# Kernel tuning notes

Hardware: AMD Instinct MI355X
Metric: run time of the kernel (lower is better)

The kernel has to match this reference:

```python
import jax, jax.numpy as jnp
import numpy as np

N = 1_000_000
C = 64
H = Wd = 2048
EPS = 1e-5


def _build_neighbors(seed=0):
    """Active-site neighbor map for a 3x3 submanifold conv on an HxW grid.
    Returns int32 [N, 9]; entry = index of active neighbor site, or -1."""
    rng = np.random.default_rng(seed)
    flat = rng.permutation(H * Wd)[:N]            # unique active coords
    grid = np.full(H * Wd, -1, np.int64)
    grid[flat] = np.arange(N)
    ys, xs = flat // Wd, flat % Wd
    cols = []
    for dy in (-1, 0, 1):
        for dx in (-1, 0, 1):
            ny, nx = ys + dy, xs + dx
            valid = (ny >= 0) & (ny < H) & (nx >= 0) & (nx < Wd)
            nf = np.where(valid, np.clip(ny, 0, H - 1) * Wd + np.clip(nx, 0, Wd - 1), 0)
            nb = np.where(valid, grid[nf], -1)    # -1 also if neighbor inactive
            cols.append(nb)
    return np.stack(cols, axis=1).astype(np.int32)


def setup_inputs() -> dict:
    key = jax.random.key(0)
    k1, k2, k3 = jax.random.split(key, 3)
    scale = 1.0 / np.sqrt(9 * C)
    return {
        "features": jax.random.normal(k1, (N, C), jnp.float32),
        "neighbor": jnp.asarray(_build_neighbors()),
        "W1": jax.random.normal(k2, (9, C, C), jnp.float32) * scale,
        "gamma1": jnp.ones((C,), jnp.float32),
        "beta1": jnp.zeros((C,), jnp.float32),
        "W2": jax.random.normal(k3, (9, C, C), jnp.float32) * scale,
        "gamma2": jnp.ones((C,), jnp.float32),
        "beta2": jnp.zeros((C,), jnp.float32),
    }


def _subm_conv(f, W, neighbor):
    # gather -> per-tap GEMM -> accumulate (submanifold: outputs only at active sites)
    out = jnp.zeros_like(f)
    for k in range(9):
        idx = neighbor[:, k]
        mask = (idx >= 0)
        g = jnp.where(mask[:, None], f[jnp.maximum(idx, 0)], 0.0)  # [N, C]
        out = out + g @ W[k]
    return out


def _bn(f, gamma, beta):
    # BatchNorm1d over the active-site axis (training-mode batch statistics)
    m = f.mean(axis=0)
    v = f.var(axis=0)
    return (f - m) * jax.lax.rsqrt(v + EPS) * gamma + beta


def reference(features, neighbor, W1, gamma1, beta1, W2, gamma2, beta2):
    out = _subm_conv(features, W1, neighbor)
    out = jax.nn.relu(_bn(out, gamma1, beta1))
    out = _subm_conv(out, W2, neighbor)
    out = _bn(out, gamma2, beta2) + features
    return jax.nn.relu(out)
```

## Files before the change

kernel.cpp:

```cpp
#include <hip/hip_runtime.h>

#define NSITES 1000000
#define CCH 64
#define EPS_BN 1e-5f

typedef __bf16 bf16x8 __attribute__((ext_vector_type(8)));
typedef float f32x4 __attribute__((ext_vector_type(4)));
typedef unsigned short ushort_t;

__device__ __forceinline__ unsigned short f2bf(float x) {
    __bf16 h = (__bf16)x;
    return __builtin_bit_cast(unsigned short, h);
}
__device__ __forceinline__ float bf2f(unsigned short u) {
    return (float)__builtin_bit_cast(__bf16, u);
}

__global__ void cast_kernel(const float* __restrict__ f, ushort_t* __restrict__ o, int total16) {
    int stride = gridDim.x * blockDim.x;
    for (int i = blockIdx.x * blockDim.x + threadIdx.x; i < total16; i += stride) {
        const float4* fp = (const float4*)(f + (size_t)i * 16);
        float4 v0 = fp[0];
        float4 v1 = fp[1];
        float4 v2 = fp[2];
        float4 v3 = fp[3];
        uint4 pa, pb;
        ushort_t* up = (ushort_t*)&pa;
        up[0] = f2bf(v0.x); up[1] = f2bf(v0.y); up[2] = f2bf(v0.z); up[3] = f2bf(v0.w);
        up[4] = f2bf(v1.x); up[5] = f2bf(v1.y); up[6] = f2bf(v1.z); up[7] = f2bf(v1.w);
        ushort_t* uq = (ushort_t*)&pb;
        uq[0] = f2bf(v2.x); uq[1] = f2bf(v2.y); uq[2] = f2bf(v2.z); uq[3] = f2bf(v2.w);
        uq[4] = f2bf(v3.x); uq[5] = f2bf(v3.y); uq[6] = f2bf(v3.z); uq[7] = f2bf(v3.w);
        uint4* op = (uint4*)(o + (size_t)i * 16);
        op[0] = pa;
        op[1] = pb;
    }
}

__global__ void swizzle_kernel(const float* __restrict__ W1, const float* __restrict__ W2,
                               ushort_t* __restrict__ W1s, ushort_t* __restrict__ W2s) {
    int t = blockIdx.x * blockDim.x + threadIdx.x;
    const float* Wg = W1;
    ushort_t* dst = W1s;
    int u = t;
    if (t >= 36864) { Wg = W2; dst = W2s; u = t - 36864; }
    int j = u & 7;
    int lane = (u >> 3) & 63;
    int nt = (u >> 9) & 3;
    int kk = (u >> 11) & 1;
    int tap = u >> 12;
    int k = 32 * kk + 8 * (lane >> 4) + j;
    int n = 16 * nt + (lane & 15);
    dst[u] = f2bf(Wg[tap * 4096 + k * 64 + n]);
}

__device__ __forceinline__ void gatherA(const ushort_t* __restrict__ fin,
                                        const int (&idxr)[2][9], int t, int quad,
                                        uint4 (&dst)[2][2]) {
#pragma unroll
    for (int mt = 0; mt < 2; ++mt) {
        int id = idxr[mt][t];
        int r = (id < 0) ? NSITES : id;
        const uint4* p = (const uint4*)(fin + ((size_t)r << 6) + (quad << 3));
        dst[mt][0] = p[0];
        dst[mt][1] = p[4];
    }
}

__device__ __forceinline__ void loadB(const ushort_t* __restrict__ Wsw, int t, int kk, int lane,
                                      bf16x8 (&B)[4]) {
#pragma unroll
    for (int nt = 0; nt < 4; ++nt)
        B[nt] = *(const bf16x8*)(Wsw + (size_t)(((t * 2 + kk) * 4 + nt) * 64 + lane) * 8);
}

template <bool OUT_BF16>
__global__ __launch_bounds__(256) void conv_kernel(
    const ushort_t* __restrict__ fin,
    const int* __restrict__ nbr,
    const ushort_t* __restrict__ Wsw,
    ushort_t* __restrict__ out_bf, float* __restrict__ out_f,
    float* __restrict__ s_sum, float* __restrict__ s_sq) {

    __shared__ float bs_sum[64];
    __shared__ float bs_sq[64];

    const int tid  = threadIdx.x;
    const int wv   = tid >> 6;
    const int lane = tid & 63;
    const int quad = lane >> 4;
    const int l15  = lane & 15;
    const int sbase = blockIdx.x * 128 + wv * 32;

    if (tid < 64) { bs_sum[tid] = 0.f; bs_sq[tid] = 0.f; }
    __syncthreads();

    int idxr[2][9];
#pragma unroll
    for (int mt = 0; mt < 2; ++mt) {
        int s = sbase + mt * 16 + l15;
        int sc = (s < NSITES) ? s : 0;
        bool sv = (s < NSITES);
#pragma unroll
        for (int t = 0; t < 9; ++t) {
            int id = nbr[(size_t)sc * 9 + t];
            idxr[mt][t] = sv ? id : -1;
        }
    }

    f32x4 acc[2][4];
#pragma unroll
    for (int mt = 0; mt < 2; ++mt)
#pragma unroll
        for (int nt = 0; nt < 4; ++nt) acc[mt][nt] = (f32x4){0.f, 0.f, 0.f, 0.f};

    uint4 abuf[3][2][2];
    gatherA(fin, idxr, 0, quad, abuf[0]);
    gatherA(fin, idxr, 1, quad, abuf[1]);

    bf16x8 B0[4];
    loadB(Wsw, 0, 0, lane, B0);

#pragma unroll
    for (int t = 0; t < 9; ++t) {
        bf16x8 B1[4];
        loadB(Wsw, t, 1, lane, B1);

        if (t < 7) gatherA(fin, idxr, t + 2, quad, abuf[(t + 2) % 3]);

        bf16x8 B0n[4];
        if (t < 8) loadB(Wsw, t + 1, 0, lane, B0n);

        __builtin_amdgcn_s_setprio(1);
#pragma unroll
        for (int mt = 0; mt < 2; ++mt) {
            bf16x8 a0 = __builtin_bit_cast(bf16x8, abuf[t % 3][mt][0]);
#pragma unroll
            for (int nt = 0; nt < 4; ++nt)
                acc[mt][nt] = __builtin_amdgcn_mfma_f32_16x16x32_bf16(a0, B0[nt], acc[mt][nt], 0, 0, 0);
        }
#pragma unroll
        for (int mt = 0; mt < 2; ++mt) {
            bf16x8 a1 = __builtin_bit_cast(bf16x8, abuf[t % 3][mt][1]);
#pragma unroll
            for (int nt = 0; nt < 4; ++nt)
                acc[mt][nt] = __builtin_amdgcn_mfma_f32_16x16x32_bf16(a1, B1[nt], acc[mt][nt], 0, 0, 0);
        }
        __builtin_amdgcn_s_setprio(0);

        if (t < 8) {
#pragma unroll
            for (int nt = 0; nt < 4; ++nt) B0[nt] = B0n[nt];
        }
    }

    float ss[4] = {0.f, 0.f, 0.f, 0.f};
    float sq[4] = {0.f, 0.f, 0.f, 0.f};
#pragma unroll
    for (int mt = 0; mt < 2; ++mt)
#pragma unroll
        for (int nt = 0; nt < 4; ++nt)
#pragma unroll
            for (int r = 0; r < 4; ++r) {
                float v = acc[mt][nt][r];
                ss[nt] += v;
                sq[nt] += v * v;
            }
#pragma unroll
    for (int nt = 0; nt < 4; ++nt) {
        ss[nt] += __shfl_xor(ss[nt], 16);
        ss[nt] += __shfl_xor(ss[nt], 32);
        sq[nt] += __shfl_xor(sq[nt], 16);
        sq[nt] += __shfl_xor(sq[nt], 32);
    }
    if (lane < 16) {
#pragma unroll
        for (int nt = 0; nt < 4; ++nt) {
            atomicAdd(&bs_sum[nt * 16 + l15], ss[nt]);
            atomicAdd(&bs_sq[nt * 16 + l15], sq[nt]);
        }
    }

    if constexpr (OUT_BF16) {
        __shared__ ushort_t tr[4 * 32 * 72];
        ushort_t* w_tr = tr + wv * 32 * 72;
#pragma unroll
        for (int mt = 0; mt < 2; ++mt)
#pragma unroll
            for (int nt = 0; nt < 4; ++nt)
#pragma unroll
                for (int r = 0; r < 4; ++r)
                    w_tr[(mt * 16 + 4 * quad + r) * 72 + nt * 16 + l15] = f2bf(acc[mt][nt][r]);
        int site_s = lane >> 1;
        int half = lane & 1;
        int gs = sbase + site_s;
        if (gs < NSITES) {
#pragma unroll
            for (int c = 0; c < 4; ++c) {
                uint4 d = *(const uint4*)(w_tr + site_s * 72 + half * 32 + c * 8);
                *(uint4*)(out_bf + (size_t)gs * 64 + half * 32 + c * 8) = d;
            }
        }
    } else {
#pragma unroll
        for (int mt = 0; mt < 2; ++mt)
#pragma unroll
            for (int nt = 0; nt < 4; ++nt)
#pragma unroll
                for (int r = 0; r < 4; ++r) {
                    int site = sbase + mt * 16 + 4 * quad + r;
                    if (site < NSITES)
                        out_f[(size_t)site * 64 + nt * 16 + l15] = acc[mt][nt][r];
                }
    }

    __syncthreads();
    if (tid < 64) {
        atomicAdd(&s_sum[tid], bs_sum[tid]);
        atomicAdd(&s_sq[tid], bs_sq[tid]);
    }
}

__global__ void finalize_kernel(const float* __restrict__ sum, const float* __restrict__ sq,
                                const float* __restrict__ gamma, const float* __restrict__ beta,
                                float* __restrict__ a, float* __restrict__ b) {
    int c = threadIdx.x;
    const float invn = 1.0f / (float)NSITES;
    float m = sum[c] * invn;
    float v = sq[c] * invn - m * m;
    float s = gamma[c] * rsqrtf(v + EPS_BN);
    a[c] = s;
    b[c] = beta[c] - m * s;
}

__global__ void act_kernel(ushort_t* __restrict__ h, const float* __restrict__ a,
                           const float* __restrict__ b, int total16) {
    int stride = gridDim.x * blockDim.x;
    for (int i = blockIdx.x * blockDim.x + threadIdx.x; i < total16; i += stride) {
        int c16 = (i & 3) * 16;
        uint4* hp = (uint4*)(h + (size_t)i * 16);
        uint4 v0 = hp[0];
        uint4 v1 = hp[1];
        float av[16], bv[16];
#pragma unroll
        for (int q = 0; q < 4; ++q) {
            *(float4*)&av[q * 4] = *(const float4*)(a + c16 + q * 4);
            *(float4*)&bv[q * 4] = *(const float4*)(b + c16 + q * 4);
        }
        ushort_t* up = (ushort_t*)&v0;
#pragma unroll
        for (int j = 0; j < 8; ++j) {
            float x = bf2f(up[j]);
            up[j] = f2bf(fmaxf(av[j] * x + bv[j], 0.f));
        }
        ushort_t* uq = (ushort_t*)&v1;
#pragma unroll
        for (int j = 0; j < 8; ++j) {
            float x = bf2f(uq[j]);
            uq[j] = f2bf(fmaxf(av[8 + j] * x + bv[8 + j], 0.f));
        }
        hp[0] = v0;
        hp[1] = v1;
    }
}

__global__ void residual_kernel(float* __restrict__ out, const float* __restrict__ feat,
                                const float* __restrict__ a2, const float* __restrict__ b2,
                                int total8) {
    int stride = gridDim.x * blockDim.x;
    for (int i = blockIdx.x * blockDim.x + threadIdx.x; i < total8; i += stride) {
        float4* op = (float4*)(out + (size_t)i * 8);
        const float4* fp = (const float4*)(feat + (size_t)i * 8);
        float4 h0 = op[0];
        float4 h1v = op[1];
        float4 f0 = fp[0];
        float4 f1 = fp[1];
        int c8 = (i & 7) * 8;
        float4 av0 = *(const float4*)(a2 + c8);
        float4 av1 = *(const float4*)(a2 + c8 + 4);
        float4 bv0 = *(const float4*)(b2 + c8);
        float4 bv1 = *(const float4*)(b2 + c8 + 4);
        float4 r0, r1;
        r0.x = fmaxf(av0.x * h0.x + bv0.x + f0.x, 0.f);
        r0.y = fmaxf(av0.y * h0.y + bv0.y + f0.y, 0.f);
        r0.z = fmaxf(av0.z * h0.z + bv0.z + f0.z, 0.f);
        r0.w = fmaxf(av0.w * h0.w + bv0.w + f0.w, 0.f);
        r1.x = fmaxf(av1.x * h1v.x + bv1.x + f1.x, 0.f);
        r1.y = fmaxf(av1.y * h1v.y + bv1.y + f1.y, 0.f);
        r1.z = fmaxf(av1.z * h1v.z + bv1.z + f1.z, 0.f);
        r1.w = fmaxf(av1.w * h1v.w + bv1.w + f1.w, 0.f);
        op[0] = r0;
        op[1] = r1;
    }
}

extern "C" void kernel_launch(void* const* d_in, const int* in_sizes, int n_in,
                              void* d_out, int out_size, void* d_ws, size_t ws_size,
                              hipStream_t stream) {
    const float* features = (const float*)d_in[0];
    const int* nbr        = (const int*)d_in[1];
    const float* W1       = (const float*)d_in[2];
    const float* gamma1   = (const float*)d_in[3];
    const float* beta1    = (const float*)d_in[4];
    const float* W2       = (const float*)d_in[5];
    const float* gamma2   = (const float*)d_in[6];
    const float* beta2    = (const float*)d_in[7];

    char* ws = (char*)d_ws;
    const size_t NB = (size_t)NSITES * CCH * sizeof(unsigned short);

    ushort_t* fbf = (ushort_t*)d_out;
    ushort_t* h1  = (ushort_t*)ws;
    size_t off = NB + 512;
    ushort_t* W1s = (ushort_t*)(ws + off);
    ushort_t* W2s = (ushort_t*)(ws + off + 147456);
    float* stats  = (float*)(ws + off + 294912);
    float* ab     = (float*)(ws + off + 294912 + 1024);

    hipMemsetAsync(stats, 0, 256 * sizeof(float), stream);
    hipMemsetAsync(fbf + (size_t)NSITES * 64, 0, 128, stream);
    hipMemsetAsync(h1 + (size_t)NSITES * 64, 0, 128, stream);

    cast_kernel<<<8192, 256, 0, stream>>>(features, fbf, NSITES * CCH / 16);
    swizzle_kernel<<<288, 256, 0, stream>>>(W1, W2, W1s, W2s);

    const int nblk = (NSITES + 127) / 128;
    conv_kernel<true><<<nblk, 256, 0, stream>>>(
        fbf, nbr, W1s, h1, nullptr, stats + 0, stats + 64);
    finalize_kernel<<<1, 64, 0, stream>>>(stats + 0, stats + 64, gamma1, beta1, ab + 0, ab + 64);

    act_kernel<<<8192, 256, 0, stream>>>(h1, ab + 0, ab + 64, NSITES * CCH / 16);

    conv_kernel<false><<<nblk, 256, 0, stream>>>(
        h1, nbr, W2s, nullptr, (float*)d_out, stats + 128, stats + 192);
    finalize_kernel<<<1, 64, 0, stream>>>(stats + 128, stats + 192, gamma2, beta2, ab + 128, ab + 192);

    residual_kernel<<<8192, 256, 0, stream>>>((float*)d_out, features, ab + 128, ab + 192,
                                              NSITES * CCH / 8);
}
```

Before: 1.099 ms.

## Fuse BN1+ReLU into second conv gather and merge prep/finalize kernels

```diff
diff --git a/kernel.cpp b/kernel.cpp
--- a/kernel.cpp
+++ b/kernel.cpp
@@ -3,6 +3,7 @@
 #define NSITES 1000000
 #define CCH 64
 #define EPS_BN 1e-5f
+#define INV_N (1.0f / 1000000.0f)
 
 typedef __bf16 bf16x8 __attribute__((ext_vector_type(8)));
 typedef float f32x4 __attribute__((ext_vector_type(4)));
@@ -16,9 +17,40 @@
     return (float)__builtin_bit_cast(__bf16, u);
 }
 
-__global__ void cast_kernel(const float* __restrict__ f, ushort_t* __restrict__ o, int total16) {
+__device__ __forceinline__ unsigned int actu32(unsigned int u, float a0, float b0,
+                                               float a1, float b1) {
+    float x0 = __builtin_bit_cast(float, u << 16);
+    float x1 = __builtin_bit_cast(float, u & 0xffff0000u);
+    float y0 = fmaxf(a0 * x0 + b0, 0.f);
+    float y1 = fmaxf(a1 * x1 + b1, 0.f);
+    return (unsigned int)f2bf(y0) | ((unsigned int)f2bf(y1) << 16);
+}
+
+__global__ void prep_kernel(const float* __restrict__ f, ushort_t* __restrict__ o,
+                            const float* __restrict__ W1, const float* __restrict__ W2,
+                            ushort_t* __restrict__ W1s, ushort_t* __restrict__ W2s,
+                            float* __restrict__ stats, int total16) {
+    int gtid = blockIdx.x * blockDim.x + threadIdx.x;
+    if (gtid < 73728) {
+        const float* Wg = W1;
+        ushort_t* dst = W1s;
+        int u = gtid;
+        if (u >= 36864) { Wg = W2; dst = W2s; u -= 36864; }
+        int j = u & 7;
+        int lane = (u >> 3) & 63;
+        int nt = (u >> 9) & 3;
+        int kk = (u >> 11) & 1;
+        int tap = u >> 12;
+        int k = 32 * kk + 8 * (lane >> 4) + j;
+        int n = 16 * nt + (lane & 15);
+        dst[u] = f2bf(Wg[tap * 4096 + k * 64 + n]);
+    } else if (gtid < 73984) {
+        stats[gtid - 73728] = 0.f;
+    } else if (gtid < 74016) {
+        ((unsigned int*)(o + (size_t)NSITES * 64))[gtid - 73984] = 0u;
+    }
     int stride = gridDim.x * blockDim.x;
-    for (int i = blockIdx.x * blockDim.x + threadIdx.x; i < total16; i += stride) {
+    for (int i = gtid; i < total16; i += stride) {
         const float4* fp = (const float4*)(f + (size_t)i * 16);
         float4 v0 = fp[0];
         float4 v1 = fp[1];
@@ -37,53 +69,33 @@
     }
 }
 
-__global__ void swizzle_kernel(const float* __restrict__ W1, const float* __restrict__ W2,
-                               ushort_t* __restrict__ W1s, ushort_t* __restrict__ W2s) {
-    int t = blockIdx.x * blockDim.x + threadIdx.x;
-    const float* Wg = W1;
-    ushort_t* dst = W1s;
-    int u = t;
-    if (t >= 36864) { Wg = W2; dst = W2s; u = t - 36864; }
-    int j = u & 7;
-    int lane = (u >> 3) & 63;
-    int nt = (u >> 9) & 3;
-    int kk = (u >> 11) & 1;
-    int tap = u >> 12;
-    int k = 32 * kk + 8 * (lane >> 4) + j;
-    int n = 16 * nt + (lane & 15);
-    dst[u] = f2bf(Wg[tap * 4096 + k * 64 + n]);
-}
-
 __device__ __forceinline__ void gatherA(const ushort_t* __restrict__ fin,
                                         const int (&idxr)[2][9], int t, int quad,
-                                        uint4 (&dst)[2][2]) {
+                                        uint4 (&dst)[2][2], int fallback) {
 #pragma unroll
     for (int mt = 0; mt < 2; ++mt) {
         int id = idxr[mt][t];
-        int r = (id < 0) ? NSITES : id;
+        int r = (id < 0) ? fallback : id;
         const uint4* p = (const uint4*)(fin + ((size_t)r << 6) + (quad << 3));
         dst[mt][0] = p[0];
         dst[mt][1] = p[4];
     }
 }
 
-__device__ __forceinline__ void loadB(const ushort_t* __restrict__ Wsw, int t, int kk, int lane,
-                                      bf16x8 (&B)[4]) {
-#pragma unroll
-    for (int nt = 0; nt < 4; ++nt)
-        B[nt] = *(const bf16x8*)(Wsw + (size_t)(((t * 2 + kk) * 4 + nt) * 64 + lane) * 8);
-}
-
-template <bool OUT_BF16>
-__global__ __launch_bounds__(256) void conv_kernel(
+template <bool OUT_BF16, bool FUSE_ACT>
+__global__ __launch_bounds__(256, 4) void conv_kernel(
     const ushort_t* __restrict__ fin,
     const int* __restrict__ nbr,
     const ushort_t* __restrict__ Wsw,
+    const float* __restrict__ p_sum, const float* __restrict__ p_sq,
+    const float* __restrict__ p_gamma, const float* __restrict__ p_beta,
     ushort_t* __restrict__ out_bf, float* __restrict__ out_f,
     float* __restrict__ s_sum, float* __restrict__ s_sq) {
 
     __shared__ float bs_sum[64];
     __shared__ float bs_sq[64];
+    __shared__ __align__(16) float s_a[64];
+    __shared__ __align__(16) float s_b[64];
 
     const int tid  = threadIdx.x;
     const int wv   = tid >> 6;
@@ -92,8 +104,29 @@
     const int l15  = lane & 15;
     const int sbase = blockIdx.x * 128 + wv * 32;
 
-    if (tid < 64) { bs_sum[tid] = 0.f; bs_sq[tid] = 0.f; }
+    if (tid < 64) {
+        bs_sum[tid] = 0.f;
+        bs_sq[tid] = 0.f;
+        if constexpr (FUSE_ACT) {
+            float m = p_sum[tid] * INV_N;
+            float v = p_sq[tid] * INV_N - m * m;
+            float s = p_gamma[tid] * rsqrtf(v + EPS_BN);
+            s_a[tid] = s;
+            s_b[tid] = p_beta[tid] - m * s;
+        }
+    }
     __syncthreads();
+
+    float af[16], bfv[16];
+    if constexpr (FUSE_ACT) {
+#pragma unroll
+        for (int j = 0; j < 8; ++j) {
+            af[j]      = s_a[quad * 8 + j];
+            af[8 + j]  = s_a[32 + quad * 8 + j];
+            bfv[j]     = s_b[quad * 8 + j];
+            bfv[8 + j] = s_b[32 + quad * 8 + j];
+        }
+    }
 
     int idxr[2][9];
 #pragma unroll
@@ -114,44 +147,55 @@
 #pragma unroll
         for (int nt = 0; nt < 4; ++nt) acc[mt][nt] = (f32x4){0.f, 0.f, 0.f, 0.f};
 
-    uint4 abuf[3][2][2];
-    gatherA(fin, idxr, 0, quad, abuf[0]);
-    gatherA(fin, idxr, 1, quad, abuf[1]);
-
-    bf16x8 B0[4];
-    loadB(Wsw, 0, 0, lane, B0);
+    constexpr int FB = FUSE_ACT ? 0 : NSITES;
+
+    uint4 abuf[2][2][2];
+    gatherA(fin, idxr, 0, quad, abuf[0], FB);
 
 #pragma unroll
     for (int t = 0; t < 9; ++t) {
-        bf16x8 B1[4];
-        loadB(Wsw, t, 1, lane, B1);
-
-        if (t < 7) gatherA(fin, idxr, t + 2, quad, abuf[(t + 2) % 3]);
-
-        bf16x8 B0n[4];
-        if (t < 8) loadB(Wsw, t + 1, 0, lane, B0n);
+        bf16x8 B[2][4];
+#pragma unroll
+        for (int kk = 0; kk < 2; ++kk)
+#pragma unroll
+            for (int nt = 0; nt < 4; ++nt)
+                B[kk][nt] = *(const bf16x8*)(Wsw + (size_t)(((t * 2 + kk) * 4 + nt) * 64 + lane) * 8);
+
+        if (t < 8) gatherA(fin, idxr, t + 1, quad, abuf[(t + 1) & 1], FB);
+
+        bf16x8 afr[2][2];
+#pragma unroll
+        for (int mt = 0; mt < 2; ++mt) {
+            uint4 r0 = abuf[t & 1][mt][0];
+            uint4 r1 = abuf[t & 1][mt][1];
+            if constexpr (FUSE_ACT) {
+                bool inv = idxr[mt][t] < 0;
+                unsigned int* p0 = (unsigned int*)&r0;
+                unsigned int* p1 = (unsigned int*)&r1;
+#pragma unroll
+                for (int p = 0; p < 4; ++p) {
+                    unsigned int t0 = actu32(p0[p], af[2 * p], bfv[2 * p],
+                                             af[2 * p + 1], bfv[2 * p + 1]);
+                    unsigned int t1 = actu32(p1[p], af[8 + 2 * p], bfv[8 + 2 * p],
+                                             af[8 + 2 * p + 1], bfv[8 + 2 * p + 1]);
+                    p0[p] = inv ? 0u : t0;
+                    p1[p] = inv ? 0u : t1;
+                }
+            }
+            afr[mt][0] = __builtin_bit_cast(bf16x8, r0);
+            afr[mt][1] = __builtin_bit_cast(bf16x8, r1);
+        }
 
         __builtin_amdgcn_s_setprio(1);
 #pragma unroll
         for (int mt = 0; mt < 2; ++mt) {
-            bf16x8 a0 = __builtin_bit_cast(bf16x8, abuf[t % 3][mt][0]);
-#pragma unroll
-            for (int nt = 0; nt < 4; ++nt)
-                acc[mt][nt] = __builtin_amdgcn_mfma_f32_16x16x32_bf16(a0, B0[nt], acc[mt][nt], 0, 0, 0);
-        }
-#pragma unroll
-        for (int mt = 0; mt < 2; ++mt) {
-            bf16x8 a1 = __builtin_bit_cast(bf16x8, abuf[t % 3][mt][1]);
-#pragma unroll
-            for (int nt = 0; nt < 4; ++nt)
-                acc[mt][nt] = __builtin_amdgcn_mfma_f32_16x16x32_bf16(a1, B1[nt], acc[mt][nt], 0, 0, 0);
+#pragma unroll
+            for (int nt = 0; nt < 4; ++nt) {
+                acc[mt][nt] = __builtin_amdgcn_mfma_f32_16x16x32_bf16(afr[mt][0], B[0][nt], acc[mt][nt], 0, 0, 0);
+                acc[mt][nt] = __builtin_amdgcn_mfma_f32_16x16x32_bf16(afr[mt][1], B[1][nt], acc[mt][nt], 0, 0, 0);
+            }
         }
         __builtin_amdgcn_s_setprio(0);
-
-        if (t < 8) {
-#pragma unroll
-            for (int nt = 0; nt < 4; ++nt) B0[nt] = B0n[nt];
-        }
     }
 
     float ss[4] = {0.f, 0.f, 0.f, 0.f};
@@ -221,52 +265,21 @@
     }
 }
 
-__global__ void finalize_kernel(const float* __restrict__ sum, const float* __restrict__ sq,
-                                const float* __restrict__ gamma, const float* __restrict__ beta,
-                                float* __restrict__ a, float* __restrict__ b) {
-    int c = threadIdx.x;
-    const float invn = 1.0f / (float)NSITES;
-    float m = sum[c] * invn;
-    float v = sq[c] * invn - m * m;
-    float s = gamma[c] * rsqrtf(v + EPS_BN);
-    a[c] = s;
-    b[c] = beta[c] - m * s;
-}
-
-__global__ void act_kernel(ushort_t* __restrict__ h, const float* __restrict__ a,
-                           const float* __restrict__ b, int total16) {
-    int stride = gridDim.x * blockDim.x;
-    for (int i = blockIdx.x * blockDim.x + threadIdx.x; i < total16; i += stride) {
-        int c16 = (i & 3) * 16;
-        uint4* hp = (uint4*)(h + (size_t)i * 16);
-        uint4 v0 = hp[0];
-        uint4 v1 = hp[1];
-        float av[16], bv[16];
-#pragma unroll
-        for (int q = 0; q < 4; ++q) {
-            *(float4*)&av[q * 4] = *(const float4*)(a + c16 + q * 4);
-            *(float4*)&bv[q * 4] = *(const float4*)(b + c16 + q * 4);
-        }
-        ushort_t* up = (ushort_t*)&v0;
-#pragma unroll
-        for (int j = 0; j < 8; ++j) {
-            float x = bf2f(up[j]);
-            up[j] = f2bf(fmaxf(av[j] * x + bv[j], 0.f));
-        }
-        ushort_t* uq = (ushort_t*)&v1;
-#pragma unroll
-        for (int j = 0; j < 8; ++j) {
-            float x = bf2f(uq[j]);
-            uq[j] = f2bf(fmaxf(av[8 + j] * x + bv[8 + j], 0.f));
-        }
-        hp[0] = v0;
-        hp[1] = v1;
-    }
-}
-
 __global__ void residual_kernel(float* __restrict__ out, const float* __restrict__ feat,
-                                const float* __restrict__ a2, const float* __restrict__ b2,
+                                const float* __restrict__ sum2, const float* __restrict__ sq2,
+                                const float* __restrict__ gamma2, const float* __restrict__ beta2,
                                 int total8) {
+    __shared__ __align__(16) float sa[64];
+    __shared__ __align__(16) float sb[64];
+    if (threadIdx.x < 64) {
+        int c = threadIdx.x;
+        float m = sum2[c] * INV_N;
+        float v = sq2[c] * INV_N - m * m;
+        float s = gamma2[c] * rsqrtf(v + EPS_BN);
+        sa[c] = s;
+        sb[c] = beta2[c] - m * s;
+    }
+    __syncthreads();
     int stride = gridDim.x * blockDim.x;
     for (int i = blockIdx.x * blockDim.x + threadIdx.x; i < total8; i += stride) {
         float4* op = (float4*)(out + (size_t)i * 8);
@@ -276,10 +289,10 @@
         float4 f0 = fp[0];
         float4 f1 = fp[1];
         int c8 = (i & 7) * 8;
-        float4 av0 = *(const float4*)(a2 + c8);
-        float4 av1 = *(const float4*)(a2 + c8 + 4);
-        float4 bv0 = *(const float4*)(b2 + c8);
-        float4 bv1 = *(const float4*)(b2 + c8 + 4);
+        float4 av0 = *(const float4*)&sa[c8];
+        float4 av1 = *(const float4*)&sa[c8 + 4];
+        float4 bv0 = *(const float4*)&sb[c8];
+        float4 bv1 = *(const float4*)&sb[c8 + 4];
         float4 r0, r1;
         r0.x = fmaxf(av0.x * h0.x + bv0.x + f0.x, 0.f);
         r0.y = fmaxf(av0.y * h0.y + bv0.y + f0.y, 0.f);
@@ -315,26 +328,20 @@
     ushort_t* W1s = (ushort_t*)(ws + off);
     ushort_t* W2s = (ushort_t*)(ws + off + 147456);
     float* stats  = (float*)(ws + off + 294912);
-    float* ab     = (float*)(ws + off + 294912 + 1024);
-
-    hipMemsetAsync(stats, 0, 256 * sizeof(float), stream);
-    hipMemsetAsync(fbf + (size_t)NSITES * 64, 0, 128, stream);
-    hipMemsetAsync(h1 + (size_t)NSITES * 64, 0, 128, stream);
-
-    cast_kernel<<<8192, 256, 0, stream>>>(features, fbf, NSITES * CCH / 16);
-    swizzle_kernel<<<288, 256, 0, stream>>>(W1, W2, W1s, W2s);
+
+    prep_kernel<<<8192, 256, 0, stream>>>(features, fbf, W1, W2, W1s, W2s, stats,
+                                          NSITES * CCH / 16);
 
     const int nblk = (NSITES + 127) / 128;
-    conv_kernel<true><<<nblk, 256, 0, stream>>>(
-        fbf, nbr, W1s, h1, nullptr, stats + 0, stats + 64);
-    finalize_kernel<<<1, 64, 0, stream>>>(stats + 0, stats + 64, gamma1, beta1, ab + 0, ab + 64);
-
-    act_kernel<<<8192, 256, 0, stream>>>(h1, ab + 0, ab + 64, NSITES * CCH / 16);
-
-    conv_kernel<false><<<nblk, 256, 0, stream>>>(
-        h1, nbr, W2s, nullptr, (float*)d_out, stats + 128, stats + 192);
-    finalize_kernel<<<1, 64, 0, stream>>>(stats + 128, stats + 192, gamma2, beta2, ab + 128, ab + 192);
-
-    residual_kernel<<<8192, 256, 0, stream>>>((float*)d_out, features, ab + 128, ab + 192,
+    conv_kernel<true, false><<<nblk, 256, 0, stream>>>(
+        fbf, nbr, W1s, nullptr, nullptr, nullptr, nullptr,
+        h1, nullptr, stats + 0, stats + 64);
+
+    conv_kernel<false, true><<<nblk, 256, 0, stream>>>(
+        h1, nbr, W2s, stats + 0, stats + 64, gamma1, beta1,
+        nullptr, (float*)d_out, stats + 128, stats + 192);
+
+    residual_kernel<<<8192, 256, 0, stream>>>((float*)d_out, features,
+                                              stats + 128, stats + 192, gamma2, beta2,
                                               NSITES * CCH / 8);
 }
```

After: 1.443 ms. 31.3% more time.
